# Kernel tuning notes

Hardware: AMD Instinct MI355X
Metric: run time of the kernel (lower is better)

Reference implementation:

```python
import jax, jax.numpy as jnp
import numpy as np

H = 512          # size_half
K = 16           # n_segments
B = 8192         # batch
WIDTH = 1.0 / K  # spline bin width


def setup_inputs() -> dict:
    key = jax.random.key(0)
    ks = jax.random.split(key, 4)
    v_in = jax.random.uniform(ks[0], (B, 2 * H), dtype=jnp.float32)  # config in [0,1]
    log_density = jax.random.normal(ks[1], (B, 1), dtype=jnp.float32)
    W1 = jax.random.normal(ks[2], (H, H), dtype=jnp.float32) * (1.0 / np.sqrt(H))
    b1 = jnp.zeros((H,), dtype=jnp.float32)
    W2 = jax.random.normal(ks[3], (H, H * K), dtype=jnp.float32) * (1.0 / np.sqrt(H))
    b2 = jnp.zeros((H * K,), dtype=jnp.float32)
    return {"v_in": v_in, "log_density": log_density, "W1": W1, "b1": b1, "W2": W2, "b2": b2}


def reference(v_in, log_density, W1, b1, W2, b2):
    # even_sites=True: passive = first half, active = second half
    v_passive = v_in[:, :H]           # [B, H]
    v_active = v_in[:, H:]            # [B, H]

    # FullyConnectedNeuralNetwork: hidden layer + final layer, tanh activation on both
    h = jnp.tanh((v_passive - 0.5) @ W1 + b1)          # [B, H]
    net = jnp.tanh(h @ W2 + b2).reshape(-1, H, K)      # [B, H, K]
    p = jax.nn.softmax(net, axis=2)                    # bin probability masses P_k

    # y-coordinates of knots: CDF of the bin masses, with leading zero
    knots_y = jnp.concatenate(
        [jnp.zeros((p.shape[0], H, 1), p.dtype), jnp.cumsum(p, axis=2)], axis=2
    )                                                  # [B, H, K+1]

    # searchsorted on uniform knots linspace(0,1,K+1), then -1, clamped
    knots_x = jnp.linspace(0.0, 1.0, K + 1, dtype=v_in.dtype)
    k = jnp.clip(jnp.searchsorted(knots_x, v_active, side="left") - 1, 0, K - 1)  # [B, H]

    p_k = jnp.take_along_axis(p, k[..., None], axis=2)[..., 0]        # [B, H]
    y_lo = jnp.take_along_axis(knots_y, k[..., None], axis=2)[..., 0]  # [B, H]

    alpha = (v_active - k.astype(v_in.dtype) * WIDTH) / WIDTH          # [B, H]
    v_out_active = y_lo + alpha * p_k

    v_out = jnp.concatenate([v_passive, v_out_active], axis=1)         # [B, 2H]
    log_density_out = log_density - jnp.sum(jnp.log(p_k), axis=1, keepdims=True)  # [B, 1]
    return v_out, log_density_out
```

## Files before the change

### kernel.cpp

```cpp
#include <hip/hip_runtime.h>
#include <hip/hip_bf16.h>

#define HH   512
#define BB   8192
#define WIDTH (1.0f/16.0f)

typedef __attribute__((ext_vector_type(8))) short  short8;
typedef __attribute__((ext_vector_type(4))) float  floatx4;

typedef const __attribute__((address_space(1))) void* gptr_t;
typedef __attribute__((address_space(3))) void*       lptr_t;

__device__ __forceinline__ void gload_lds16(const void* g, void* l) {
    __builtin_amdgcn_global_load_lds((gptr_t)g, (lptr_t)l, 16, 0, 0);
}

__device__ __forceinline__ float tanh_fast(float x) {
    float e = __expf(2.0f * x);
    return 1.0f - 2.0f * __builtin_amdgcn_rcpf(e + 1.0f);
}

__global__ void prep_v(const float* __restrict__ vin,
                       float* __restrict__ vout,
                       __hip_bfloat16* __restrict__ Abf) {
    int i = blockIdx.x * 256 + threadIdx.x;
    int b = i >> 6, c = i & 63;
    const float4* src = (const float4*)(vin + (size_t)b * 1024 + c * 8);
    float4 f0 = src[0], f1 = src[1];
    float4* dst = (float4*)(vout + (size_t)b * 1024 + c * 8);
    dst[0] = f0; dst[1] = f1;
    union { __hip_bfloat16 h[8]; uint4 v; } u;
    u.h[0] = __float2bfloat16(f0.x - 0.5f); u.h[1] = __float2bfloat16(f0.y - 0.5f);
    u.h[2] = __float2bfloat16(f0.z - 0.5f); u.h[3] = __float2bfloat16(f0.w - 0.5f);
    u.h[4] = __float2bfloat16(f1.x - 0.5f); u.h[5] = __float2bfloat16(f1.y - 0.5f);
    u.h[6] = __float2bfloat16(f1.z - 0.5f); u.h[7] = __float2bfloat16(f1.w - 0.5f);
    *(uint4*)(Abf + (size_t)b * 512 + c * 8) = u.v;
}

__global__ void transpose_f32_bf16(const float* __restrict__ src,
                                   __hip_bfloat16* __restrict__ dst,
                                   int rows, int cols) {
    __shared__ float tile[32][33];
    int c0 = blockIdx.x * 32, r0 = blockIdx.y * 32;
    int x = threadIdx.x, y = threadIdx.y;
    #pragma unroll
    for (int i = 0; i < 32; i += 8)
        tile[y + i][x] = src[(size_t)(r0 + y + i) * cols + c0 + x];
    __syncthreads();
    #pragma unroll
    for (int i = 0; i < 32; i += 8)
        dst[(size_t)(c0 + y + i) * rows + r0 + x] = __float2bfloat16(tile[x][y + i]);
}

__global__ __launch_bounds__(256, 4) void gemm1_kernel(
        const __hip_bfloat16* __restrict__ Abf,
        const __hip_bfloat16* __restrict__ W1T,
        const float* __restrict__ b1,
        __hip_bfloat16* __restrict__ hM) {
    __shared__ short ldsA[64 * 32];
    __shared__ short ldsB[128 * 32];
    int tid = threadIdx.x;
    int lane = tid & 63;
    int wv = tid >> 6, wr = wv >> 1, wc = wv & 1;
    int q = lane >> 4, cx = lane & 15;
    int rowBase = blockIdx.y * 64;
    int colBase = blockIdx.x * 128;
    floatx4 acc[2][4] = {};

    for (int k0 = 0; k0 < HH; k0 += 32) {
        {
            int row = tid >> 2, kc = tid & 3;
            unsigned loff = __builtin_amdgcn_readfirstlane((unsigned)((tid & 192) * 16));
            gload_lds16(Abf + (size_t)(rowBase + row) * HH + k0 + kc * 8, (char*)ldsA + loff);
        }
        #pragma unroll
        for (int j = 0; j < 2; ++j) {
            int i = j * 256 + tid;
            int row = i >> 2, kc = i & 3;
            unsigned loff = __builtin_amdgcn_readfirstlane((unsigned)((j * 256 + (tid & 192)) * 16));
            gload_lds16(W1T + (size_t)(colBase + row) * HH + k0 + kc * 8, (char*)ldsB + loff);
        }
        __syncthreads();
        short8 a[2], b[4];
        #pragma unroll
        for (int mt = 0; mt < 2; ++mt)
            a[mt] = *(const short8*)(ldsA + (wr * 32 + mt * 16 + cx) * 32 + q * 8);
        #pragma unroll
        for (int nt = 0; nt < 4; ++nt)
            b[nt] = *(const short8*)(ldsB + (wc * 64 + nt * 16 + cx) * 32 + q * 8);
        #pragma unroll
        for (int mt = 0; mt < 2; ++mt)
            #pragma unroll
            for (int nt = 0; nt < 4; ++nt)
                acc[mt][nt] = __builtin_amdgcn_mfma_f32_16x16x32_bf16(a[mt], b[nt], acc[mt][nt], 0, 0, 0);
        __syncthreads();
    }

    float b1v[4];
    #pragma unroll
    for (int nt = 0; nt < 4; ++nt) b1v[nt] = b1[colBase + wc * 64 + nt * 16 + cx];
    #pragma unroll
    for (int mt = 0; mt < 2; ++mt)
        #pragma unroll
        for (int nt = 0; nt < 4; ++nt) {
            int col = colBase + wc * 64 + nt * 16 + cx;
            #pragma unroll
            for (int r = 0; r < 4; ++r) {
                int row = rowBase + wr * 32 + mt * 16 + q * 4 + r;
                hM[(size_t)row * HH + col] = __float2bfloat16(tanh_fast(acc[mt][nt][r] + b1v[nt]));
            }
        }
}

__global__ __launch_bounds__(256, 4) void gemm2_kernel(
        const __hip_bfloat16* __restrict__ hM,
        const __hip_bfloat16* __restrict__ W2T,
        const float* __restrict__ b2,
        const float* __restrict__ vin,
        float* __restrict__ vout,
        float* __restrict__ partial) {
    __shared__ __align__(16) char smem[32768];
    short* ldsA = (short*)smem;
    short* ldsB = (short*)(smem + 16384);
    float* ldsE = (float*)smem;
    int tid = threadIdx.x;
    int lane = tid & 63;
    int wv = tid >> 6, wr = wv >> 1, wc = wv & 1;
    int q = lane >> 4, cx = lane & 15;
    int rowBase = blockIdx.y * 128;
    int colBase = blockIdx.x * 128;
    floatx4 acc[4][4] = {};

    for (int k0 = 0; k0 < HH; k0 += 64) {
        #pragma unroll
        for (int j = 0; j < 4; ++j) {
            int chunk = j * 256 + tid;
            int half  = j >> 1;
            int c2    = chunk & 511;
            int row = c2 >> 2, kc = c2 & 3;
            unsigned loff = __builtin_amdgcn_readfirstlane((unsigned)((j * 256 + (tid & 192)) * 16));
            gload_lds16(hM  + (size_t)(rowBase + row) * HH + k0 + half * 32 + kc * 8, (char*)ldsA + loff);
            gload_lds16(W2T + (size_t)(colBase + row) * HH + k0 + half * 32 + kc * 8, (char*)ldsB + loff);
        }
        __syncthreads();
        #pragma unroll
        for (int s = 0; s < 2; ++s) {
            const short* pA = ldsA + s * 4096;
            const short* pB = ldsB + s * 4096;
            short8 a[4], b[4];
            #pragma unroll
            for (int mt = 0; mt < 4; ++mt)
                a[mt] = *(const short8*)(pA + (wr * 64 + mt * 16 + cx) * 32 + q * 8);
            #pragma unroll
            for (int nt = 0; nt < 4; ++nt)
                b[nt] = *(const short8*)(pB + (wc * 64 + nt * 16 + cx) * 32 + q * 8);
            #pragma unroll
            for (int mt = 0; mt < 4; ++mt)
                #pragma unroll
                for (int nt = 0; nt < 4; ++nt)
                    acc[mt][nt] = __builtin_amdgcn_mfma_f32_16x16x32_bf16(a[mt], b[nt], acc[mt][nt], 0, 0, 0);
        }
        __syncthreads();
    }

    float b2v[4];
    #pragma unroll
    for (int nt = 0; nt < 4; ++nt) b2v[nt] = b2[colBase + wc * 64 + nt * 16 + cx];

    float* myTile = ldsE + wv * (16 * 68);
    int rowL  = lane & 15;
    int gL    = lane >> 4;
    int gAbs  = blockIdx.x * 8 + wc * 4 + gL;

    #pragma unroll
    for (int mt = 0; mt < 4; ++mt) {
        #pragma unroll
        for (int nt = 0; nt < 4; ++nt)
            #pragma unroll
            for (int r = 0; r < 4; ++r)
                myTile[(q * 4 + r) * 68 + nt * 16 + cx] = acc[mt][nt][r] + b2v[nt];

        floatx4 x0 = *(const floatx4*)(myTile + rowL * 68 + gL * 16);
        floatx4 x1 = *(const floatx4*)(myTile + rowL * 68 + gL * 16 + 4);
        floatx4 x2 = *(const floatx4*)(myTile + rowL * 68 + gL * 16 + 8);
        floatx4 x3 = *(const floatx4*)(myTile + rowL * 68 + gL * 16 + 12);
        float xs[16] = { x0[0],x0[1],x0[2],x0[3], x1[0],x1[1],x1[2],x1[3],
                         x2[0],x2[1],x2[2],x2[3], x3[0],x3[1],x3[2],x3[3] };

        int row = rowBase + wr * 64 + mt * 16 + rowL;
        float v = vin[(size_t)row * 1024 + 512 + gAbs];
        int k = (int)ceilf(v * 16.0f) - 1;
        k = min(15, max(0, k));

        float s = 0.0f, csum = 0.0f, ek = 0.0f;
        #pragma unroll
        for (int j = 0; j < 16; ++j) {
            float e2 = __expf(2.0f * xs[j]);
            float t  = 1.0f - 2.0f * __builtin_amdgcn_rcpf(e2 + 1.0f);
            float e  = __expf(t);
            csum += (j < k)  ? e : 0.0f;
            ek    = (j == k) ? e : ek;
            s += e;
        }
        float rs = __builtin_amdgcn_rcpf(s);
        float pk  = ek * rs;
        float ylo = csum * rs;
        float alpha = (v - (float)k * WIDTH) * 16.0f;
        vout[(size_t)row * 1024 + 512 + gAbs] = ylo + alpha * pk;

        float logp = __logf(pk);
        logp += __shfl_xor(logp, 16, 64);
        logp += __shfl_xor(logp, 32, 64);
        if (lane < 16) partial[(size_t)row * 128 + blockIdx.x * 2 + wc] = logp;
    }
}

__global__ void finish_logdens(const float* __restrict__ partial,
                               const float* __restrict__ ld,
                               float* __restrict__ out) {
    int wv = threadIdx.x >> 6, lane = threadIdx.x & 63;
    int row = blockIdx.x * 4 + wv;
    float s = partial[(size_t)row * 128 + lane] + partial[(size_t)row * 128 + 64 + lane];
    #pragma unroll
    for (int d = 32; d > 0; d >>= 1) s += __shfl_down(s, d, 64);
    if (lane == 0) out[row] = ld[row] - s;
}

extern "C" void kernel_launch(void* const* d_in, const int* in_sizes, int n_in,
                              void* d_out, int out_size, void* d_ws, size_t ws_size,
                              hipStream_t stream) {
    const float* vin = (const float*)d_in[0];
    const float* ld  = (const float*)d_in[1];
    const float* W1  = (const float*)d_in[2];
    const float* b1  = (const float*)d_in[3];
    const float* W2  = (const float*)d_in[4];
    const float* b2  = (const float*)d_in[5];
    float* vout  = (float*)d_out;
    float* ldout = vout + (size_t)BB * 1024;

    char* ws = (char*)d_ws;
    __hip_bfloat16* Abf = (__hip_bfloat16*)(ws);
    __hip_bfloat16* W1T = (__hip_bfloat16*)(ws + 8388608);
    __hip_bfloat16* W2T = (__hip_bfloat16*)(ws + 8912896);
    __hip_bfloat16* hM  = (__hip_bfloat16*)(ws + 17301504);
    float* partial = (float*)(ws + 25690112);

    transpose_f32_bf16<<<dim3(16, 16),  dim3(32, 8), 0, stream>>>(W1, W1T, 512, 512);
    transpose_f32_bf16<<<dim3(256, 16), dim3(32, 8), 0, stream>>>(W2, W2T, 512, 8192);
    prep_v<<<2048, 256, 0, stream>>>(vin, vout, Abf);
    gemm1_kernel<<<dim3(4, 128), 256, 0, stream>>>(Abf, W1T, b1, hM);
    gemm2_kernel<<<dim3(64, 64), 256, 0, stream>>>(hM, W2T, b2, vin, vout, partial);
    finish_logdens<<<2048, 256, 0, stream>>>(partial, ld, ldout);
}
```

Baseline: 211.4 us.

## Merge prep kernels, swizzle gemm2 LDS layout, fold log-density reduction into atomics

The two weight transposes and the input prep now run as one kernel launch, which also copies log_density into the output. gemm2's LDS tiles are XOR-swizzled on the k-chunk index so that the MFMA operand reads avoid bank conflicts. The separate finish kernel and the partial buffer are removed, and gemm2 atomically subtracts its per-block log-probability sums directly into the output. This saves two launches and a round trip through the partial buffer, in exchange for float atomics with nondeterministic summation order.

Result: no change. 207.4 us (-1.9%).

```diff
diff --git a/kernel.cpp b/kernel.cpp
--- a/kernel.cpp
+++ b/kernel.cpp
@@ -20,36 +20,42 @@
     return 1.0f - 2.0f * __builtin_amdgcn_rcpf(e + 1.0f);
 }
 
-__global__ void prep_v(const float* __restrict__ vin,
-                       float* __restrict__ vout,
-                       __hip_bfloat16* __restrict__ Abf) {
-    int i = blockIdx.x * 256 + threadIdx.x;
-    int b = i >> 6, c = i & 63;
-    const float4* src = (const float4*)(vin + (size_t)b * 1024 + c * 8);
-    float4 f0 = src[0], f1 = src[1];
-    float4* dst = (float4*)(vout + (size_t)b * 1024 + c * 8);
-    dst[0] = f0; dst[1] = f1;
-    union { __hip_bfloat16 h[8]; uint4 v; } u;
-    u.h[0] = __float2bfloat16(f0.x - 0.5f); u.h[1] = __float2bfloat16(f0.y - 0.5f);
-    u.h[2] = __float2bfloat16(f0.z - 0.5f); u.h[3] = __float2bfloat16(f0.w - 0.5f);
-    u.h[4] = __float2bfloat16(f1.x - 0.5f); u.h[5] = __float2bfloat16(f1.y - 0.5f);
-    u.h[6] = __float2bfloat16(f1.z - 0.5f); u.h[7] = __float2bfloat16(f1.w - 0.5f);
-    *(uint4*)(Abf + (size_t)b * 512 + c * 8) = u.v;
-}
-
-__global__ void transpose_f32_bf16(const float* __restrict__ src,
-                                   __hip_bfloat16* __restrict__ dst,
-                                   int rows, int cols) {
+__global__ void prep_all(const float* __restrict__ vin, const float* __restrict__ W1,
+                         const float* __restrict__ W2, const float* __restrict__ ld,
+                         float* __restrict__ vout, float* __restrict__ ldout,
+                         __hip_bfloat16* __restrict__ Abf,
+                         __hip_bfloat16* __restrict__ W1T,
+                         __hip_bfloat16* __restrict__ W2T) {
     __shared__ float tile[32][33];
-    int c0 = blockIdx.x * 32, r0 = blockIdx.y * 32;
-    int x = threadIdx.x, y = threadIdx.y;
-    #pragma unroll
-    for (int i = 0; i < 32; i += 8)
-        tile[y + i][x] = src[(size_t)(r0 + y + i) * cols + c0 + x];
-    __syncthreads();
-    #pragma unroll
-    for (int i = 0; i < 32; i += 8)
-        dst[(size_t)(c0 + y + i) * rows + r0 + x] = __float2bfloat16(tile[x][y + i]);
+    int bid = blockIdx.x, tid = threadIdx.x;
+    if (bid < 4352) {
+        const float* src;  __hip_bfloat16* dst;  int cols, c0, r0;
+        if (bid < 4096) { src = W2; dst = W2T; cols = 8192; c0 = (bid & 255) * 32; r0 = (bid >> 8) * 32; }
+        else            { int b = bid - 4096; src = W1; dst = W1T; cols = 512; c0 = (b & 15) * 32; r0 = (b >> 4) * 32; }
+        int x = tid & 31, y = tid >> 5;
+        #pragma unroll
+        for (int i = 0; i < 32; i += 8)
+            tile[y + i][x] = src[(size_t)(r0 + y + i) * cols + c0 + x];
+        __syncthreads();
+        #pragma unroll
+        for (int i = 0; i < 32; i += 8)
+            dst[(size_t)(c0 + y + i) * 512 + r0 + x] = __float2bfloat16(tile[x][y + i]);
+    } else {
+        int b = bid - 4352;
+        int i = b * 256 + tid;
+        int r = i >> 6, c = i & 63;
+        const float4* src = (const float4*)(vin + (size_t)r * 1024 + c * 8);
+        float4 f0 = src[0], f1 = src[1];
+        float4* dst = (float4*)(vout + (size_t)r * 1024 + c * 8);
+        dst[0] = f0; dst[1] = f1;
+        union { __hip_bfloat16 h[8]; uint4 v; } u;
+        u.h[0] = __float2bfloat16(f0.x - 0.5f); u.h[1] = __float2bfloat16(f0.y - 0.5f);
+        u.h[2] = __float2bfloat16(f0.z - 0.5f); u.h[3] = __float2bfloat16(f0.w - 0.5f);
+        u.h[4] = __float2bfloat16(f1.x - 0.5f); u.h[5] = __float2bfloat16(f1.y - 0.5f);
+        u.h[6] = __float2bfloat16(f1.z - 0.5f); u.h[7] = __float2bfloat16(f1.w - 0.5f);
+        *(uint4*)(Abf + (size_t)r * 512 + c * 8) = u.v;
+        if (tid < 4) { int row = b * 4 + tid; ldout[row] = ld[row]; }
+    }
 }
 
 __global__ __launch_bounds__(256, 4) void gemm1_kernel(
@@ -118,7 +124,7 @@
         const float* __restrict__ b2,
         const float* __restrict__ vin,
         float* __restrict__ vout,
-        float* __restrict__ partial) {
+        float* __restrict__ ldout) {
     __shared__ __align__(16) char smem[32768];
     short* ldsA = (short*)smem;
     short* ldsB = (short*)(smem + 16384);
@@ -131,6 +137,8 @@
     int colBase = blockIdx.x * 128;
     floatx4 acc[4][4] = {};
 
+    int aoff = (q ^ (cx & 3)) * 8;
+
     for (int k0 = 0; k0 < HH; k0 += 64) {
         #pragma unroll
         for (int j = 0; j < 4; ++j) {
@@ -138,9 +146,10 @@
             int half  = j >> 1;
             int c2    = chunk & 511;
             int row = c2 >> 2, kc = c2 & 3;
+            int kcs = kc ^ (row & 3);
             unsigned loff = __builtin_amdgcn_readfirstlane((unsigned)((j * 256 + (tid & 192)) * 16));
-            gload_lds16(hM  + (size_t)(rowBase + row) * HH + k0 + half * 32 + kc * 8, (char*)ldsA + loff);
-            gload_lds16(W2T + (size_t)(colBase + row) * HH + k0 + half * 32 + kc * 8, (char*)ldsB + loff);
+            gload_lds16(hM  + (size_t)(rowBase + row) * HH + k0 + half * 32 + kcs * 8, (char*)ldsA + loff);
+            gload_lds16(W2T + (size_t)(colBase + row) * HH + k0 + half * 32 + kcs * 8, (char*)ldsB + loff);
         }
         __syncthreads();
         #pragma unroll
@@ -150,10 +159,10 @@
             short8 a[4], b[4];
             #pragma unroll
             for (int mt = 0; mt < 4; ++mt)
-                a[mt] = *(const short8*)(pA + (wr * 64 + mt * 16 + cx) * 32 + q * 8);
+                a[mt] = *(const short8*)(pA + (wr * 64 + mt * 16 + cx) * 32 + aoff);
             #pragma unroll
             for (int nt = 0; nt < 4; ++nt)
-                b[nt] = *(const short8*)(pB + (wc * 64 + nt * 16 + cx) * 32 + q * 8);
+                b[nt] = *(const short8*)(pB + (wc * 64 + nt * 16 + cx) * 32 + aoff);
             #pragma unroll
             for (int mt = 0; mt < 4; ++mt)
                 #pragma unroll
@@ -211,19 +220,8 @@
         float logp = __logf(pk);
         logp += __shfl_xor(logp, 16, 64);
         logp += __shfl_xor(logp, 32, 64);
-        if (lane < 16) partial[(size_t)row * 128 + blockIdx.x * 2 + wc] = logp;
-    }
-}
-
-__global__ void finish_logdens(const float* __restrict__ partial,
-                               const float* __restrict__ ld,
-                               float* __restrict__ out) {
-    int wv = threadIdx.x >> 6, lane = threadIdx.x & 63;
-    int row = blockIdx.x * 4 + wv;
-    float s = partial[(size_t)row * 128 + lane] + partial[(size_t)row * 128 + 64 + lane];
-    #pragma unroll
-    for (int d = 32; d > 0; d >>= 1) s += __shfl_down(s, d, 64);
-    if (lane == 0) out[row] = ld[row] - s;
+        if (lane < 16) atomicAdd(ldout + row, -logp);
+    }
 }
 
 extern "C" void kernel_launch(void* const* d_in, const int* in_sizes, int n_in,
@@ -243,12 +241,8 @@
     __hip_bfloat16* W1T = (__hip_bfloat16*)(ws + 8388608);
     __hip_bfloat16* W2T = (__hip_bfloat16*)(ws + 8912896);
     __hip_bfloat16* hM  = (__hip_bfloat16*)(ws + 17301504);
-    float* partial = (float*)(ws + 25690112);
-
-    transpose_f32_bf16<<<dim3(16, 16),  dim3(32, 8), 0, stream>>>(W1, W1T, 512, 512);
-    transpose_f32_bf16<<<dim3(256, 16), dim3(32, 8), 0, stream>>>(W2, W2T, 512, 8192);
-    prep_v<<<2048, 256, 0, stream>>>(vin, vout, Abf);
+
+    prep_all<<<6400, 256, 0, stream>>>(vin, W1, W2, ld, vout, ldout, Abf, W1T, W2T);
     gemm1_kernel<<<dim3(4, 128), 256, 0, stream>>>(Abf, W1T, b1, hM);
-    gemm2_kernel<<<dim3(64, 64), 256, 0, stream>>>(hM, W2T, b2, vin, vout, partial);
-    finish_logdens<<<2048, 256, 0, stream>>>(partial, ld, ldout);
-}
+    gemm2_kernel<<<dim3(64, 64), 256, 0, stream>>>(hM, W2T, b2, vin, vout, ldout);
+}
```
